# Kernel tuning notes

Hardware: AMD Instinct MI355X
Metric: run time of the kernel (lower is better)

Reference implementation:

```python
import jax, jax.numpy as jnp
import numpy as np

EPS = 1e-6


def softmax_kernel_transformation(data, is_query, projection_matrix):
    # data: [B,L,H,D], projection_matrix: [M,D]
    d = data.shape[-1]
    m = projection_matrix.shape[0]
    data_normalizer = 1.0 / jnp.sqrt(jnp.sqrt(jnp.float32(d)))
    data = data_normalizer * data
    ratio = 1.0 / jnp.sqrt(jnp.float32(m))
    data_dash = jnp.einsum('blhd,md->blhm', data, projection_matrix)
    diag_data = jnp.sum(jnp.square(data), axis=-1, keepdims=True) / 2.0  # [B,L,H,1]
    if is_query:
        stab = jnp.max(data_dash, axis=-1, keepdims=True)  # per-position max over M
    else:
        stab = jnp.max(data_dash, axis=(1, 3), keepdims=True)  # max over L and M
    return ratio * (jnp.exp(data_dash - diag_data - stab) + EPS)


def causal_linear_attention(qp, kp, v):
    # qp,kp: [L,B,H,M]; v: [L,B,H,D]. Sequential prefix-sum recurrence (FAVOR+ causal).
    B, H, M = qp.shape[1], qp.shape[2], qp.shape[3]
    D = v.shape[-1]
    kv0 = jnp.zeros((B, H, M, D), dtype=v.dtype)
    ks0 = jnp.zeros((B, H, M), dtype=kp.dtype)

    def step(carry, inp):
        kv_sum, k_sum = carry
        q_t, k_t, v_t = inp  # [B,H,M], [B,H,M], [B,H,D]
        kv_sum = kv_sum + jnp.einsum('bhm,bhd->bhmd', k_t, v_t)
        k_sum = k_sum + k_t
        num_t = jnp.einsum('bhmd,bhm->bhd', kv_sum, q_t)  # numerator row
        den_t = jnp.einsum('bhm,bhm->bh', q_t, k_sum)     # normalizer row
        return (kv_sum, k_sum), (num_t, den_t)

    (_, _), (num, den) = jax.lax.scan(step, (kv0, ks0), (qp, kp, v))
    return num, den  # [L,B,H,D], [L,B,H]


def favor_attention(query, key, value, projection_matrix):
    query_prime = softmax_kernel_transformation(query, True, projection_matrix)   # [B,L,H,M]
    key_prime = softmax_kernel_transformation(key, False, projection_matrix)      # [B,L,H,M]
    qp = jnp.transpose(query_prime, (1, 0, 2, 3))  # [L,B,H,M]
    kp = jnp.transpose(key_prime, (1, 0, 2, 3))
    v = jnp.transpose(value, (1, 0, 2, 3))         # [L,B,H,D]
    num, den = causal_linear_attention(qp, kp, v)
    av = jnp.transpose(num, (1, 0, 2, 3))          # [B,L,H,D]
    norm = jnp.transpose(den, (1, 0, 2))[..., None]  # [B,L,H,1]
    return av / norm


def setup_inputs() -> dict:
    B, L, H, D, M = 2, 2048, 8, 64, 128
    root = jax.random.key(0)
    kq, kk, kv, kp = jax.random.split(root, 4)
    return {
        'query': jax.random.normal(kq, (B, L, H, D), dtype=jnp.float32),
        'key': jax.random.normal(kk, (B, L, H, D), dtype=jnp.float32),
        'value': jax.random.normal(kv, (B, L, H, D), dtype=jnp.float32),
        'projection_matrix': jax.random.normal(kp, (M, D), dtype=jnp.float32),
    }


def reference(query, key, value, projection_matrix):
    return favor_attention(query, key, value, projection_matrix)
```

## Files before the change

### kernel.cpp

```cpp
#include <hip/hip_runtime.h>
#include <math.h>

typedef __attribute__((ext_vector_type(8))) short short8;
typedef __attribute__((ext_vector_type(4))) float f32x4;
typedef __attribute__((ext_vector_type(4))) unsigned short u16x4;

constexpr int B_ = 2, L_ = 2048, H_ = 8, D_ = 64, M_ = 128;
constexpr int T_ = 64;
constexpr int C_ = L_ / T_;
constexpr float DN_ = 0.35355339059327373f;
constexpr float RATIO_ = 0.08838834764831845f;
constexpr float EPSV_ = 1e-6f;
constexpr float REPS_ = RATIO_ * EPSV_;
constexpr float KEPS_ = 64.0f * REPS_;

__device__ inline unsigned short f2bf(float x) {
  const unsigned u = __float_as_uint(x);
  return (unsigned short)((u + 0x7fffu + ((u >> 16) & 1u)) >> 16);
}
__device__ inline float bf2f(unsigned short h) {
  return __uint_as_float(((unsigned)h) << 16);
}

constexpr int FXK_ = 0, FPH_ = 4608, FVT_ = 13824;
constexpr int FKPT_ = 4608, FKVST_ = 4608;

__global__ __launch_bounds__(256, 4) void feat_kernel(
    const float* __restrict__ k, const float* __restrict__ P,
    const float* __restrict__ v, unsigned short* __restrict__ kvc16,
    float* __restrict__ ksc, unsigned short* __restrict__ vt16,
    float* __restrict__ blockmax, float* __restrict__ vsum) {
  __shared__ __align__(16) unsigned short sm[18432];
  __shared__ float diagk_s[T_];
  __shared__ float red4_s[4];

  const int sub = blockIdx.x;
  const int c = sub % C_, bh = sub / C_;
  const int b = bh >> 3, h = bh & 7;
  const int tid = threadIdx.x;
  const int w = tid >> 6, lane = tid & 63;
  const int l15 = lane & 15, l16 = lane >> 4;
  const int rblk = (w >> 1) * 32, cblk = (w & 1) * 64;

#pragma unroll
  for (int it = 0; it < 4; ++it) {
    const int i4 = tid + 256 * it;
    const int r = i4 >> 4, d0 = (i4 & 15) * 4;
    f32x4 t4 = *reinterpret_cast<const f32x4*>(
        &k[((size_t)(b * L_ + c * T_ + r) * H_ + h) * D_ + d0]);
    u16x4 hi;
    float sq = 0.f;
#pragma unroll
    for (int j = 0; j < 4; ++j) {
      const float xv = t4[j] * DN_;
      sq += xv * xv;
      hi[j] = f2bf(xv);
    }
    *reinterpret_cast<u16x4*>(&sm[FXK_ + r * 72 + d0]) = hi;
#pragma unroll
    for (int off = 1; off < 16; off <<= 1) sq += __shfl_xor(sq, off, 64);
    if ((tid & 15) == 0) diagk_s[r] = sq;
  }
  for (int i4 = tid; i4 < M_ * 16; i4 += 256) {
    const int m = i4 >> 4, d0 = (i4 & 15) * 4;
    const f32x4 t4 = *reinterpret_cast<const f32x4*>(&P[m * D_ + d0]);
    u16x4 hi;
#pragma unroll
    for (int j = 0; j < 4; ++j) hi[j] = f2bf(t4[j]);
    *reinterpret_cast<u16x4*>(&sm[FPH_ + m * 72 + d0]) = hi;
  }
#pragma unroll
  for (int it = 0; it < 4; ++it) {
    const int i4 = tid + 256 * it;
    const int t = i4 >> 4, d0 = (i4 & 15) * 4;
    const f32x4 t4 = *reinterpret_cast<const f32x4*>(
        &v[((size_t)(b * L_ + c * T_ + t) * H_ + h) * D_ + d0]);
#pragma unroll
    for (int j = 0; j < 4; ++j) sm[FVT_ + (d0 + j) * 72 + t] = f2bf(t4[j]);
  }
  __syncthreads();

  f32x4 acck[2][4];
#pragma unroll
  for (int i = 0; i < 2; ++i)
#pragma unroll
    for (int j = 0; j < 4; ++j) acck[i][j] = {0.f, 0.f, 0.f, 0.f};
#pragma unroll
  for (int kk = 0; kk < 2; ++kk) {
    short8 ah[2], bh8[4];
#pragma unroll
    for (int ti = 0; ti < 2; ++ti)
      ah[ti] = *reinterpret_cast<const short8*>(
          &sm[FXK_ + (rblk + ti * 16 + l15) * 72 + kk * 32 + l16 * 8]);
#pragma unroll
    for (int tj = 0; tj < 4; ++tj)
      bh8[tj] = *reinterpret_cast<const short8*>(
          &sm[FPH_ + (cblk + tj * 16 + l15) * 72 + kk * 32 + l16 * 8]);
#pragma unroll
    for (int ti = 0; ti < 2; ++ti)
#pragma unroll
      for (int tj = 0; tj < 4; ++tj)
        acck[ti][tj] = __builtin_amdgcn_mfma_f32_16x16x32_bf16(
            ah[ti], bh8[tj], acck[ti][tj], 0, 0, 0);
  }
  {
    float bm = -INFINITY;
#pragma unroll
    for (int ti = 0; ti < 2; ++ti)
#pragma unroll
      for (int tj = 0; tj < 4; ++tj)
#pragma unroll
        for (int j = 0; j < 4; ++j) bm = fmaxf(bm, acck[ti][tj][j]);
#pragma unroll
    for (int off = 1; off < 64; off <<= 1)
      bm = fmaxf(bm, __shfl_xor(bm, off, 64));
    if (lane == 0) red4_s[w] = bm;
  }
  __syncthreads();

  const float lmax =
      fmaxf(fmaxf(red4_s[0], red4_s[1]), fmaxf(red4_s[2], red4_s[3]));
  if (tid == 0) blockmax[sub] = lmax;
#pragma unroll
  for (int ti = 0; ti < 2; ++ti)
#pragma unroll
    for (int j = 0; j < 4; ++j) {
      const int row = rblk + ti * 16 + l16 * 4 + j;
      const float sub2 = 0.5f * diagk_s[row] + lmax;
#pragma unroll
      for (int tj = 0; tj < 4; ++tj) {
        const int col = cblk + tj * 16 + l15;
        sm[FKPT_ + col * 72 + row] = f2bf(RATIO_ * expf(acck[ti][tj][j] - sub2));
      }
    }
  __syncthreads();

  f32x4 acc2[2][4];
#pragma unroll
  for (int i = 0; i < 2; ++i)
#pragma unroll
    for (int j = 0; j < 4; ++j) acc2[i][j] = {0.f, 0.f, 0.f, 0.f};
#pragma unroll
  for (int kk = 0; kk < 2; ++kk) {
    short8 av[2], bv[4];
#pragma unroll
    for (int ti = 0; ti < 2; ++ti)
      av[ti] = *reinterpret_cast<const short8*>(
          &sm[FVT_ + (rblk + ti * 16 + l15) * 72 + kk * 32 + l16 * 8]);
#pragma unroll
    for (int tj = 0; tj < 4; ++tj)
      bv[tj] = *reinterpret_cast<const short8*>(
          &sm[FKPT_ + (cblk + tj * 16 + l15) * 72 + kk * 32 + l16 * 8]);
#pragma unroll
    for (int ti = 0; ti < 2; ++ti)
#pragma unroll
      for (int tj = 0; tj < 4; ++tj)
        acc2[ti][tj] = __builtin_amdgcn_mfma_f32_16x16x32_bf16(
            av[ti], bv[tj], acc2[ti][tj], 0, 0, 0);
  }
  {
    unsigned short* vg = vt16 + (size_t)(bh * C_ + c) * (D_ * T_);
    for (int i8 = tid; i8 < D_ * 8; i8 += 256) {
      const int d = i8 >> 3, t0 = (i8 & 7) * 8;
      *reinterpret_cast<short8*>(&vg[d * T_ + t0]) =
          *reinterpret_cast<const short8*>(&sm[FVT_ + d * 72 + t0]);
    }
  }
  if (tid < M_) {
    float s = 0.f;
#pragma unroll
    for (int t8 = 0; t8 < 8; ++t8) {
      const short8 h8 =
          *reinterpret_cast<const short8*>(&sm[FKPT_ + tid * 72 + t8 * 8]);
#pragma unroll
      for (int j = 0; j < 8; ++j) s += bf2f((unsigned short)h8[j]);
    }
    ksc[(size_t)(bh * C_ + c) * M_ + tid] = s;
  }
  if (tid >= 128 && tid < 128 + D_) {
    const int d = tid - 128;
    float s = 0.f;
#pragma unroll
    for (int t8 = 0; t8 < 8; ++t8) {
      const short8 h8 =
          *reinterpret_cast<const short8*>(&sm[FVT_ + d * 72 + t8 * 8]);
#pragma unroll
      for (int j = 0; j < 8; ++j) s += bf2f((unsigned short)h8[j]);
    }
    vsum[(size_t)(bh * C_ + c) * D_ + d] = s;
  }
  __syncthreads();
#pragma unroll
  for (int ti = 0; ti < 2; ++ti)
#pragma unroll
    for (int j = 0; j < 4; ++j) {
      const int row = rblk + ti * 16 + l16 * 4 + j;
#pragma unroll
      for (int tj = 0; tj < 4; ++tj) {
        const int col = cblk + tj * 16 + l15;
        sm[FKVST_ + row * 136 + col] = f2bf(acc2[ti][tj][j]);
      }
    }
  __syncthreads();
  {
    unsigned short* ob = kvc16 + (size_t)(bh * C_ + c) * (M_ * D_);
    for (int i8 = tid; i8 < D_ * 16; i8 += 256) {
      const int d = i8 >> 4, m0 = (i8 & 15) * 8;
      *reinterpret_cast<short8*>(&ob[d * M_ + m0]) =
          *reinterpret_cast<const short8*>(&sm[FKVST_ + d * 136 + m0]);
    }
  }
}

__global__ __launch_bounds__(256) void prefix_kernel(
    const unsigned short* __restrict__ kvc16,
    unsigned short* __restrict__ kvp16, float* __restrict__ ksc,
    const float* __restrict__ blockmax, const float* __restrict__ vsum) {
  __shared__ float bm_s[C_];
  __shared__ float sc_s[C_];
  __shared__ float vs_s[2][C_];
  const int bid = blockIdx.x;
  const int ej = bid & 31, bh = bid >> 5;
  if (threadIdx.x < C_) bm_s[threadIdx.x] = blockmax[bh * C_ + threadIdx.x];
  if (threadIdx.x >= 64 && threadIdx.x < 64 + 2 * C_) {
    const int t = threadIdx.x - 64;
    const int ld = t >> 5, cc = t & 31;
    vs_s[ld][cc] = vsum[(size_t)(bh * C_ + cc) * D_ + ej * 2 + ld];
  }
  __syncthreads();
  if (threadIdx.x < C_) {
    float km = -INFINITY;
#pragma unroll
    for (int cc = 0; cc < C_; ++cc) km = fmaxf(km, bm_s[cc]);
    sc_s[threadIdx.x] = expf(bm_s[threadIdx.x] - km);
  }
  __syncthreads();
  const int e = ej * 256 + threadIdx.x;
  const int dl = threadIdx.x >> 7;
  float vals[C_];
#pragma unroll
  for (int cc = 0; cc < C_; ++cc)
    vals[cc] = bf2f(kvc16[(size_t)(bh * C_ + cc) * (M_ * D_) + e]) * sc_s[cc] +
               REPS_ * vs_s[dl][cc];
  float run = 0.f;
#pragma unroll
  for (int cc = 0; cc < C_; ++cc) {
    const float t = vals[cc];
    vals[cc] = run;
    run += t;
  }
#pragma unroll
  for (int cc = 0; cc < C_; ++cc)
    kvp16[(size_t)(bh * C_ + cc) * (M_ * D_) + e] = f2bf(vals[cc]);
  if (ej == 0 && threadIdx.x < M_) {
    const int m = threadIdx.x;
    float ks[C_];
#pragma unroll
    for (int cc = 0; cc < C_; ++cc)
      ks[cc] = ksc[(size_t)(bh * C_ + cc) * M_ + m] * sc_s[cc] + KEPS_;
    float rs = 0.f;
#pragma unroll
    for (int cc = 0; cc < C_; ++cc) {
      const float t = ks[cc];
      ks[cc] = rs;
      rs += t;
    }
#pragma unroll
    for (int cc = 0; cc < C_; ++cc)
      ksc[(size_t)(bh * C_ + cc) * M_ + m] = ks[cc];
  }
}

constexpr int IXQ_ = 0, IXK_ = 4608, IPH_ = 9216;
constexpr int IQP_ = 0, IKP_ = 9216, IS_ = 18432;

__global__ __launch_bounds__(256, 3) void intra_kernel(
    const float* __restrict__ q, const float* __restrict__ k,
    const float* __restrict__ P, const unsigned short* __restrict__ vt16,
    const unsigned short* __restrict__ kvp16, const float* __restrict__ ksp,
    const float* __restrict__ blockmax, float* __restrict__ out) {
  __shared__ __align__(16) unsigned short sm[23040];
  __shared__ float diagq_s[T_];
  __shared__ float diagk_s[T_];
  __shared__ float wred_s[2][T_];
  __shared__ float qs2_s[2][T_];
  __shared__ float ksp_s[M_];
  __shared__ float denp_s[4][T_];
  __shared__ float den_s[T_];
  __shared__ float bm_s[C_];

  const int bid = blockIdx.x;
  const int c = bid % C_, bh = bid / C_;
  const int b = bh >> 3, h = bh & 7;
  const int tid = threadIdx.x;
  const int w = tid >> 6, lane = tid & 63;
  const int l15 = lane & 15, l16 = lane >> 4;
  const int rblk = (w >> 1) * 32;
  const int cblkF = (w & 1) * 64;
  const int cblkS = (w & 1) * 32;
  const int dblk = (w & 1) * 32;

  if (tid < C_) bm_s[tid] = blockmax[bh * C_ + tid];
  if (tid < M_) ksp_s[tid] = ksp[(size_t)(bh * C_ + c) * M_ + tid];

#pragma unroll
  for (int it = 0; it < 4; ++it) {
    const int i4 = tid + 256 * it;
    const int r = i4 >> 4, d0 = (i4 & 15) * 4;
    f32x4 t4 = *reinterpret_cast<const f32x4*>(
        &q[((size_t)(b * L_ + c * T_ + r) * H_ + h) * D_ + d0]);
    u16x4 hi;
    float sq = 0.f;
#pragma unroll
    for (int j = 0; j < 4; ++j) {
      const float xv = t4[j] * DN_;
      sq += xv * xv;
      hi[j] = f2bf(xv);
    }
    *reinterpret_cast<u16x4*>(&sm[IXQ_ + r * 72 + d0]) = hi;
#pragma unroll
    for (int off = 1; off < 16; off <<= 1) sq += __shfl_xor(sq, off, 64);
    if ((tid & 15) == 0) diagq_s[r] = sq;
  }
#pragma unroll
  for (int it = 0; it < 4; ++it) {
    const int i4 = tid + 256 * it;
    const int r = i4 >> 4, d0 = (i4 & 15) * 4;
    f32x4 t4 = *reinterpret_cast<const f32x4*>(
        &k[((size_t)(b * L_ + c * T_ + r) * H_ + h) * D_ + d0]);
    u16x4 hi;
    float sq = 0.f;
#pragma unroll
    for (int j = 0; j < 4; ++j) {
      const float xv = t4[j] * DN_;
      sq += xv * xv;
      hi[j] = f2bf(xv);
    }
    *reinterpret_cast<u16x4*>(&sm[IXK_ + r * 72 + d0]) = hi;
#pragma unroll
    for (int off = 1; off < 16; off <<= 1) sq += __shfl_xor(sq, off, 64);
    if ((tid & 15) == 0) diagk_s[r] = sq;
  }
  for (int i4 = tid; i4 < M_ * 16; i4 += 256) {
    const int m = i4 >> 4, d0 = (i4 & 15) * 4;
    const f32x4 t4 = *reinterpret_cast<const f32x4*>(&P[m * D_ + d0]);
    u16x4 hi;
#pragma unroll
    for (int j = 0; j < 4; ++j) hi[j] = f2bf(t4[j]);
    *reinterpret_cast<u16x4*>(&sm[IPH_ + m * 72 + d0]) = hi;
  }
  __syncthreads();

  f32x4 accq[2][4], acck[2][4];
#pragma unroll
  for (int i = 0; i < 2; ++i)
#pragma unroll
    for (int j = 0; j < 4; ++j) {
      accq[i][j] = {0.f, 0.f, 0.f, 0.f};
      acck[i][j] = {0.f, 0.f, 0.f, 0.f};
    }
#pragma unroll
  for (int kk = 0; kk < 2; ++kk) {
    short8 aq[2], ak[2], bh8[4];
#pragma unroll
    for (int ti = 0; ti < 2; ++ti) {
      aq[ti] = *reinterpret_cast<const short8*>(
          &sm[IXQ_ + (rblk + ti * 16 + l15) * 72 + kk * 32 + l16 * 8]);
      ak[ti] = *reinterpret_cast<const short8*>(
          &sm[IXK_ + (rblk + ti * 16 + l15) * 72 + kk * 32 + l16 * 8]);
    }
#pragma unroll
    for (int tj = 0; tj < 4; ++tj)
      bh8[tj] = *reinterpret_cast<const short8*>(
          &sm[IPH_ + (cblkF + tj * 16 + l15) * 72 + kk * 32 + l16 * 8]);
#pragma unroll
    for (int ti = 0; ti < 2; ++ti)
#pragma unroll
      for (int tj = 0; tj < 4; ++tj) {
        accq[ti][tj] = __builtin_amdgcn_mfma_f32_16x16x32_bf16(
            aq[ti], bh8[tj], accq[ti][tj], 0, 0, 0);
        acck[ti][tj] = __builtin_amdgcn_mfma_f32_16x16x32_bf16(
            ak[ti], bh8[tj], acck[ti][tj], 0, 0, 0);
      }
  }
  {
    float rmax[2][4];
#pragma unroll
    for (int ti = 0; ti < 2; ++ti)
#pragma unroll
      for (int j = 0; j < 4; ++j) {
        float m0 = fmaxf(fmaxf(accq[ti][0][j], accq[ti][1][j]),
                         fmaxf(accq[ti][2][j], accq[ti][3][j]));
#pragma unroll
        for (int off = 1; off < 16; off <<= 1)
          m0 = fmaxf(m0, __shfl_xor(m0, off, 64));
        rmax[ti][j] = m0;
      }
    if (l15 == 0) {
#pragma unroll
      for (int ti = 0; ti < 2; ++ti)
#pragma unroll
        for (int j = 0; j < 4; ++j)
          wred_s[w & 1][rblk + ti * 16 + l16 * 4 + j] = rmax[ti][j];
    }
  }
  __syncthreads();

  const float lmax = bm_s[c];
#pragma unroll
  for (int ti = 0; ti < 2; ++ti)
#pragma unroll
    for (int j = 0; j < 4; ++j) {
      const int row = rblk + ti * 16 + l16 * 4 + j;
      const float subq =
          0.5f * diagq_s[row] + fmaxf(wred_s[0][row], wred_s[1][row]);
      const float subk = 0.5f * diagk_s[row] + lmax;
      float qsp = 0.f;
#pragma unroll
      for (int tj = 0; tj < 4; ++tj) {
        const int col = cblkF + tj * 16 + l15;
        const float qv = RATIO_ * (expf(accq[ti][tj][j] - subq) + EPSV_);
        qsp += qv;
        sm[IQP_ + row * 136 + col] = f2bf(qv);
        sm[IKP_ + row * 136 + col] =
            f2bf(RATIO_ * expf(acck[ti][tj][j] - subk));
      }
#pragma unroll
      for (int off = 1; off < 16; off <<= 1) qsp += __shfl_xor(qsp, off, 64);
      if (l15 == 0) qs2_s[w & 1][row] = qsp;
    }
  __syncthreads();

  const unsigned short* kvt = kvp16 + (size_t)(bh * C_ + c) * (M_ * D_);
  const unsigned short* vg = vt16 + (size_t)(bh * C_ + c) * (D_ * T_);
  short8 vtr[2][2], kvr[4][2];
#pragma unroll
  for (int kk = 0; kk < 2; ++kk)
#pragma unroll
    for (int tj = 0; tj < 2; ++tj)
      vtr[kk][tj] = *reinterpret_cast<const short8*>(
          &vg[(dblk + tj * 16 + l15) * T_ + kk * 32 + l16 * 8]);
#pragma unroll
  for (int kk = 0; kk < 4; ++kk)
#pragma unroll
    for (int tj = 0; tj < 2; ++tj)
      kvr[kk][tj] = *reinterpret_cast<const short8*>(
          &kvt[(dblk + tj * 16 + l15) * M_ + kk * 32 + l16 * 8]);

  float km = -INFINITY;
#pragma unroll
  for (int cc = 0; cc < C_; ++cc) km = fmaxf(km, bm_s[cc]);
  const float sc = expf(bm_s[c] - km);

  f32x4 Sacc[2][2];
#pragma unroll
  for (int i = 0; i < 2; ++i)
#pragma unroll
    for (int j = 0; j < 2; ++j) Sacc[i][j] = {0.f, 0.f, 0.f, 0.f};
#pragma unroll
  for (int kk = 0; kk < 4; ++kk) {
    short8 af[2], bf[2];
#pragma unroll
    for (int ti = 0; ti < 2; ++ti)
      af[ti] = *reinterpret_cast<const short8*>(
          &sm[IQP_ + (rblk + ti * 16 + l15) * 136 + kk * 32 + l16 * 8]);
#pragma unroll
    for (int tj = 0; tj < 2; ++tj)
      bf[tj] = *reinterpret_cast<const short8*>(
          &sm[IKP_ + (cblkS + tj * 16 + l15) * 136 + kk * 32 + l16 * 8]);
#pragma unroll
    for (int ti = 0; ti < 2; ++ti)
#pragma unroll
      for (int tj = 0; tj < 2; ++tj)
        Sacc[ti][tj] = __builtin_amdgcn_mfma_f32_16x16x32_bf16(
            af[ti], bf[tj], Sacc[ti][tj], 0, 0, 0);
  }
#pragma unroll
  for (int ti = 0; ti < 2; ++ti)
#pragma unroll
    for (int tj = 0; tj < 2; ++tj)
#pragma unroll
      for (int j = 0; j < 4; ++j) {
        const int row = rblk + ti * 16 + l16 * 4 + j;
        const int col = cblkS + tj * 16 + l15;
        const float add = REPS_ * (qs2_s[0][row] + qs2_s[1][row]);
        const float sv = (col <= row) ? Sacc[ti][tj][j] * sc + add : 0.f;
        sm[IS_ + row * 72 + col] = f2bf(sv);
      }
  __syncthreads();

  {
    const int t = lane;
    float p = 0.f;
    if (w == 0) {
      for (int tp = 0; tp < 32; ++tp) p += bf2f(sm[IS_ + t * 72 + tp]);
    } else if (w == 1) {
      for (int tp = 32; tp < 64; ++tp) p += bf2f(sm[IS_ + t * 72 + tp]);
    } else if (w == 2) {
      for (int m = 0; m < 64; ++m)
        p += bf2f(sm[IQP_ + t * 136 + m]) * ksp_s[m];
    } else {
      for (int m = 64; m < 128; ++m)
        p += bf2f(sm[IQP_ + t * 136 + m]) * ksp_s[m];
    }
    denp_s[w][t] = p;
  }
  __syncthreads();
  if (tid < T_)
    den_s[tid] =
        denp_s[0][tid] + denp_s[1][tid] + denp_s[2][tid] + denp_s[3][tid];
  __syncthreads();

  f32x4 Nacc[2][2];
#pragma unroll
  for (int i = 0; i < 2; ++i)
#pragma unroll
    for (int j = 0; j < 2; ++j) Nacc[i][j] = {0.f, 0.f, 0.f, 0.f};
#pragma unroll
  for (int kk = 0; kk < 2; ++kk) {
    short8 af[2];
#pragma unroll
    for (int ti = 0; ti < 2; ++ti)
      af[ti] = *reinterpret_cast<const short8*>(
          &sm[IS_ + (rblk + ti * 16 + l15) * 72 + kk * 32 + l16 * 8]);
#pragma unroll
    for (int ti = 0; ti < 2; ++ti)
#pragma unroll
      for (int tj = 0; tj < 2; ++tj)
        Nacc[ti][tj] = __builtin_amdgcn_mfma_f32_16x16x32_bf16(
            af[ti], vtr[kk][tj], Nacc[ti][tj], 0, 0, 0);
  }
#pragma unroll
  for (int kk = 0; kk < 4; ++kk) {
    short8 af[2];
#pragma unroll
    for (int ti = 0; ti < 2; ++ti)
      af[ti] = *reinterpret_cast<const short8*>(
          &sm[IQP_ + (rblk + ti * 16 + l15) * 136 + kk * 32 + l16 * 8]);
#pragma unroll
    for (int ti = 0; ti < 2; ++ti)
#pragma unroll
      for (int tj = 0; tj < 2; ++tj)
        Nacc[ti][tj] = __builtin_amdgcn_mfma_f32_16x16x32_bf16(
            af[ti], kvr[kk][tj], Nacc[ti][tj], 0, 0, 0);
  }

#pragma unroll
  for (int ti = 0; ti < 2; ++ti)
#pragma unroll
    for (int j = 0; j < 4; ++j) {
      const int row = rblk + ti * 16 + l16 * 4 + j;
      const float r = 1.f / den_s[row];
      float* orow = out + ((size_t)(b * L_ + c * T_ + row) * H_ + h) * D_;
#pragma unroll
      for (int tj = 0; tj < 2; ++tj) {
        const int col = dblk + tj * 16 + l15;
        orow[col] = Nacc[ti][tj][j] * r;
      }
    }
}

extern "C" void kernel_launch(void* const* d_in, const int* in_sizes, int n_in,
                              void* d_out, int out_size, void* d_ws,
                              size_t ws_size, hipStream_t stream) {
  const float* q = (const float*)d_in[0];
  const float* k = (const float*)d_in[1];
  const float* v = (const float*)d_in[2];
  const float* P = (const float*)d_in[3];
  float* out = (float*)d_out;

  float* ws = (float*)d_ws;
  float* blockmax = ws;
  float* ksc = blockmax + 512;
  float* vsum = ksc + (size_t)B_ * H_ * C_ * M_;
  unsigned short* kvc16 = (unsigned short*)(vsum + (size_t)B_ * H_ * C_ * D_);
  unsigned short* kvp16 = kvc16 + (size_t)B_ * H_ * C_ * D_ * M_;
  unsigned short* vt16 = kvp16 + (size_t)B_ * H_ * C_ * D_ * M_;

  feat_kernel<<<B_ * H_ * C_, 256, 0, stream>>>(k, P, v, kvc16, ksc, vt16,
                                                blockmax, vsum);
  prefix_kernel<<<B_ * H_ * 32, 256, 0, stream>>>(kvc16, kvp16, ksc, blockmax,
                                                  vsum);
  intra_kernel<<<B_ * H_ * C_, 256, 0, stream>>>(q, k, P, vt16, kvp16, ksc,
                                                 blockmax, out);
}
```

Before: 41.28 us.

## Fuse chunk prefix scan into intra kernel, dropping separate prefix kernel

Removes the prefix_kernel launch and the kvp16 intermediate buffer. Each intra_kernel block now sums the per-chunk KV states and key sums of all earlier chunks directly from kvc16/ksc, applying the max-rescale and epsilon terms inline. This saves a kernel launch and a global write/read round trip. In exchange, prefix work becomes quadratic in chunk count (chunk c reads c previous states) and is load-imbalanced across blocks.

```diff
diff --git a/kernel.cpp b/kernel.cpp
--- a/kernel.cpp
+++ b/kernel.cpp
@@ -212,73 +212,15 @@
   }
 }
 
-__global__ __launch_bounds__(256) void prefix_kernel(
-    const unsigned short* __restrict__ kvc16,
-    unsigned short* __restrict__ kvp16, float* __restrict__ ksc,
-    const float* __restrict__ blockmax, const float* __restrict__ vsum) {
-  __shared__ float bm_s[C_];
-  __shared__ float sc_s[C_];
-  __shared__ float vs_s[2][C_];
-  const int bid = blockIdx.x;
-  const int ej = bid & 31, bh = bid >> 5;
-  if (threadIdx.x < C_) bm_s[threadIdx.x] = blockmax[bh * C_ + threadIdx.x];
-  if (threadIdx.x >= 64 && threadIdx.x < 64 + 2 * C_) {
-    const int t = threadIdx.x - 64;
-    const int ld = t >> 5, cc = t & 31;
-    vs_s[ld][cc] = vsum[(size_t)(bh * C_ + cc) * D_ + ej * 2 + ld];
-  }
-  __syncthreads();
-  if (threadIdx.x < C_) {
-    float km = -INFINITY;
-#pragma unroll
-    for (int cc = 0; cc < C_; ++cc) km = fmaxf(km, bm_s[cc]);
-    sc_s[threadIdx.x] = expf(bm_s[threadIdx.x] - km);
-  }
-  __syncthreads();
-  const int e = ej * 256 + threadIdx.x;
-  const int dl = threadIdx.x >> 7;
-  float vals[C_];
-#pragma unroll
-  for (int cc = 0; cc < C_; ++cc)
-    vals[cc] = bf2f(kvc16[(size_t)(bh * C_ + cc) * (M_ * D_) + e]) * sc_s[cc] +
-               REPS_ * vs_s[dl][cc];
-  float run = 0.f;
-#pragma unroll
-  for (int cc = 0; cc < C_; ++cc) {
-    const float t = vals[cc];
-    vals[cc] = run;
-    run += t;
-  }
-#pragma unroll
-  for (int cc = 0; cc < C_; ++cc)
-    kvp16[(size_t)(bh * C_ + cc) * (M_ * D_) + e] = f2bf(vals[cc]);
-  if (ej == 0 && threadIdx.x < M_) {
-    const int m = threadIdx.x;
-    float ks[C_];
-#pragma unroll
-    for (int cc = 0; cc < C_; ++cc)
-      ks[cc] = ksc[(size_t)(bh * C_ + cc) * M_ + m] * sc_s[cc] + KEPS_;
-    float rs = 0.f;
-#pragma unroll
-    for (int cc = 0; cc < C_; ++cc) {
-      const float t = ks[cc];
-      ks[cc] = rs;
-      rs += t;
-    }
-#pragma unroll
-    for (int cc = 0; cc < C_; ++cc)
-      ksc[(size_t)(bh * C_ + cc) * M_ + m] = ks[cc];
-  }
-}
-
 constexpr int IXQ_ = 0, IXK_ = 4608, IPH_ = 9216;
 constexpr int IQP_ = 0, IKP_ = 9216, IS_ = 18432;
 
 __global__ __launch_bounds__(256, 3) void intra_kernel(
     const float* __restrict__ q, const float* __restrict__ k,
     const float* __restrict__ P, const unsigned short* __restrict__ vt16,
-    const unsigned short* __restrict__ kvp16, const float* __restrict__ ksp,
-    const float* __restrict__ blockmax, float* __restrict__ out) {
+    const unsigned short* __restrict__ kvc16, const float* __restrict__ ksc,
+    const float* __restrict__ vsum, const float* __restrict__ blockmax,
+    float* __restrict__ out) {
   __shared__ __align__(16) unsigned short sm[23040];
   __shared__ float diagq_s[T_];
   __shared__ float diagk_s[T_];
@@ -288,6 +230,7 @@
   __shared__ float denp_s[4][T_];
   __shared__ float den_s[T_];
   __shared__ float bm_s[C_];
+  __shared__ float sc_s[C_];
 
   const int bid = blockIdx.x;
   const int c = bid % C_, bh = bid / C_;
@@ -301,7 +244,6 @@
   const int dblk = (w & 1) * 32;
 
   if (tid < C_) bm_s[tid] = blockmax[bh * C_ + tid];
-  if (tid < M_) ksp_s[tid] = ksp[(size_t)(bh * C_ + c) * M_ + tid];
 
 #pragma unroll
   for (int it = 0; it < 4; ++it) {
@@ -351,6 +293,13 @@
   }
   __syncthreads();
 
+  if (tid < C_) {
+    float km = -INFINITY;
+#pragma unroll
+    for (int cc = 0; cc < C_; ++cc) km = fmaxf(km, bm_s[cc]);
+    sc_s[tid] = expf(bm_s[tid] - km);
+  }
+
   f32x4 accq[2][4], acck[2][4];
 #pragma unroll
   for (int i = 0; i < 2; ++i)
@@ -429,9 +378,14 @@
       for (int off = 1; off < 16; off <<= 1) qsp += __shfl_xor(qsp, off, 64);
       if (l15 == 0) qs2_s[w & 1][row] = qsp;
     }
-  __syncthreads();
-
-  const unsigned short* kvt = kvp16 + (size_t)(bh * C_ + c) * (M_ * D_);
+  if (tid < M_) {
+    float s = 0.f;
+    for (int cc = 0; cc < c; ++cc)
+      s += ksc[(size_t)(bh * C_ + cc) * M_ + tid] * sc_s[cc] + KEPS_;
+    ksp_s[tid] = s;
+  }
+  __syncthreads();
+
   const unsigned short* vg = vt16 + (size_t)(bh * C_ + c) * (D_ * T_);
   short8 vtr[2][2], kvr[4][2];
 #pragma unroll
@@ -441,16 +395,37 @@
       vtr[kk][tj] = *reinterpret_cast<const short8*>(
           &vg[(dblk + tj * 16 + l15) * T_ + kk * 32 + l16 * 8]);
 #pragma unroll
-  for (int kk = 0; kk < 4; ++kk)
-#pragma unroll
-    for (int tj = 0; tj < 2; ++tj)
-      kvr[kk][tj] = *reinterpret_cast<const short8*>(
-          &kvt[(dblk + tj * 16 + l15) * M_ + kk * 32 + l16 * 8]);
-
-  float km = -INFINITY;
-#pragma unroll
-  for (int cc = 0; cc < C_; ++cc) km = fmaxf(km, bm_s[cc]);
-  const float sc = expf(bm_s[c] - km);
+  for (int tj = 0; tj < 2; ++tj) {
+    const int d = dblk + tj * 16 + l15;
+    float acc8[4][8];
+#pragma unroll
+    for (int kk = 0; kk < 4; ++kk)
+#pragma unroll
+      for (int j = 0; j < 8; ++j) acc8[kk][j] = 0.f;
+    for (int cc = 0; cc < c; ++cc) {
+      const float scc = sc_s[cc];
+      const float vse = REPS_ * vsum[(size_t)(bh * C_ + cc) * D_ + d];
+      const unsigned short* kb =
+          kvc16 + (size_t)(bh * C_ + cc) * (M_ * D_) + d * M_;
+#pragma unroll
+      for (int kk = 0; kk < 4; ++kk) {
+        const short8 h8 =
+            *reinterpret_cast<const short8*>(&kb[kk * 32 + l16 * 8]);
+#pragma unroll
+        for (int j = 0; j < 8; ++j)
+          acc8[kk][j] += scc * bf2f((unsigned short)h8[j]) + vse;
+      }
+    }
+#pragma unroll
+    for (int kk = 0; kk < 4; ++kk) {
+      short8 o;
+#pragma unroll
+      for (int j = 0; j < 8; ++j) o[j] = (short)f2bf(acc8[kk][j]);
+      kvr[kk][tj] = o;
+    }
+  }
+
+  const float sc = sc_s[c];
 
   f32x4 Sacc[2][2];
 #pragma unroll
@@ -574,13 +549,10 @@
   float* ksc = blockmax + 512;
   float* vsum = ksc + (size_t)B_ * H_ * C_ * M_;
   unsigned short* kvc16 = (unsigned short*)(vsum + (size_t)B_ * H_ * C_ * D_);
-  unsigned short* kvp16 = kvc16 + (size_t)B_ * H_ * C_ * D_ * M_;
-  unsigned short* vt16 = kvp16 + (size_t)B_ * H_ * C_ * D_ * M_;
+  unsigned short* vt16 = kvc16 + (size_t)B_ * H_ * C_ * D_ * M_;
 
   feat_kernel<<<B_ * H_ * C_, 256, 0, stream>>>(k, P, v, kvc16, ksc, vt16,
                                                 blockmax, vsum);
-  prefix_kernel<<<B_ * H_ * 32, 256, 0, stream>>>(kvc16, kvp16, ksc, blockmax,
-                                                  vsum);
-  intra_kernel<<<B_ * H_ * C_, 256, 0, stream>>>(q, k, P, vt16, kvp16, ksc,
-                                                 blockmax, out);
+  intra_kernel<<<B_ * H_ * C_, 256, 0, stream>>>(q, k, P, vt16, kvc16, ksc,
+                                                 vsum, blockmax, out);
 }
```

New measurement: 93.96 us. +127.6%, slower.
